# Performance work log

Measured on AMD Instinct MI355X. Metric: run time of the kernel, lower is better.

Reference implementation:

```python
import jax, jax.numpy as jnp
import numpy as np

FEAT = 512
HEADS = 8
HEAD_DIM = FEAT // HEADS
HIDDEN = 2048
EPS = 1e-5


def _linear(x, W, b):
    # torch Linear: y = x @ W.T + b, W: (out, in)
    return jnp.einsum('bnd,od->bno', x, W) + b


def _layernorm(x, g, b):
    mu = jnp.mean(x, axis=-1, keepdims=True)
    var = jnp.var(x, axis=-1, keepdims=True)
    return (x - mu) * jax.lax.rsqrt(var + EPS) * g + b


def setup_inputs() -> dict:
    key = jax.random.key(0)
    ks = jax.random.split(key, 16)
    bsz, N = 16, 512
    gain = 2 ** (-0.5)
    lim = gain * np.sqrt(6.0 / (FEAT + FEAT))
    inp = {
        'nfeat': jax.random.normal(ks[0], (bsz, N, FEAT), jnp.float32),
        'attn_bias': jax.random.normal(ks[1], (bsz, N, N, HEADS), jnp.float32),
        'attn_mask': jax.random.randint(ks[2], (bsz, N, N), 0, 2, jnp.int32),
        'Wq': jax.random.uniform(ks[3], (FEAT, FEAT), jnp.float32, -lim, lim),
        'bq': jnp.zeros((FEAT,), jnp.float32),
        'Wk': jax.random.uniform(ks[4], (FEAT, FEAT), jnp.float32, -lim, lim),
        'bk': jnp.zeros((FEAT,), jnp.float32),
        'Wv': jax.random.uniform(ks[5], (FEAT, FEAT), jnp.float32, -lim, lim),
        'bv': jnp.zeros((FEAT,), jnp.float32),
        'Wo': jax.random.uniform(ks[6], (FEAT, FEAT), jnp.float32, -np.sqrt(6.0/(2*FEAT)), np.sqrt(6.0/(2*FEAT))),
        'bo': jnp.zeros((FEAT,), jnp.float32),
        'W1': jax.random.normal(ks[7], (HIDDEN, FEAT), jnp.float32) * 0.02,
        'b1': jnp.zeros((HIDDEN,), jnp.float32),
        'W2': jax.random.normal(ks[8], (FEAT, HIDDEN), jnp.float32) * 0.02,
        'b2': jnp.zeros((FEAT,), jnp.float32),
        'ln1_g': jnp.ones((FEAT,), jnp.float32),
        'ln1_b': jnp.zeros((FEAT,), jnp.float32),
        'ln2_g': jnp.ones((FEAT,), jnp.float32),
        'ln2_b': jnp.zeros((FEAT,), jnp.float32),
    }
    return inp


def reference(nfeat, attn_bias, attn_mask, Wq, bq, Wk, bk, Wv, bv, Wo, bo,
              W1, b1, W2, b2, ln1_g, ln1_b, ln2_g, ln2_b):
    bsz, N, _ = nfeat.shape
    residual = nfeat
    # --- biased multi-head attention (norm_first=False => no pre-norm) ---
    q = _linear(nfeat, Wq, bq).reshape(bsz, N, HEADS, HEAD_DIM)
    k = _linear(nfeat, Wk, bk).reshape(bsz, N, HEADS, HEAD_DIM)
    v = _linear(nfeat, Wv, bv).reshape(bsz, N, HEADS, HEAD_DIM)
    # NOTE: original code does q / scaling with scaling = head_dim**-0.5,
    # i.e. scores are MULTIPLIED by sqrt(head_dim) (faithful to source).
    scale = jnp.float32(HEAD_DIM ** 0.5)
    scores = jnp.einsum('bqhd,bkhd->bhqk', q, k) * scale  # (b,h,N,N)
    scores = scores + jnp.transpose(attn_bias, (0, 3, 1, 2))  # additive bias
    mask = (attn_mask != 0)[:, None, :, :]
    scores = jnp.where(mask, -jnp.inf, scores)
    attn = jax.nn.softmax(scores, axis=-1)
    ctx = jnp.einsum('bhqk,bkhd->bqhd', attn, v).reshape(bsz, N, FEAT)
    out = _linear(ctx, Wo, bo)
    x = residual + out
    x = _layernorm(x, ln1_g, ln1_b)
    # --- FFN ---
    residual = x
    h = jax.nn.relu(_linear(x, W1, b1))
    h = _linear(h, W2, b2)
    x = residual + h
    x = _layernorm(x, ln2_g, ln2_b)
    return x
```

## Files before the change

kernel.cpp:

```cpp
#include <hip/hip_runtime.h>
#include <hip/hip_bf16.h>
#include <stdint.h>

typedef unsigned short u16;
typedef __attribute__((ext_vector_type(8))) __bf16 bf16x8;
typedef __attribute__((ext_vector_type(4))) float f32x4;
typedef __attribute__((ext_vector_type(4))) unsigned short u16x4;

#define B_   16
#define N_   512
#define D_   512
#define H_   8
#define DH_  64
#define HID_ 2048
#define M_   8192
#define FRAG_BH 32768

__device__ __forceinline__ u16 f2bf(float f) {
    unsigned u = __float_as_uint(f);
    u += 0x7fffu + ((u >> 16) & 1u);
    return (u16)(u >> 16);
}
__device__ __forceinline__ float bf2f(u16 u) {
    return __uint_as_float(((unsigned)u) << 16);
}
__device__ __forceinline__ f32x4 mfma16(bf16x8 a, bf16x8 b, f32x4 c) {
    return __builtin_amdgcn_mfma_f32_16x16x32_bf16(a, b, c, 0, 0, 0);
}
__device__ __forceinline__ void gload_lds16(const u16* g, u16* l) {
    __builtin_amdgcn_global_load_lds(
        (const __attribute__((address_space(1))) void*)g,
        (__attribute__((address_space(3))) void*)l, 16, 0, 0);
}

__device__ __forceinline__ void cvt4(const float* s, u16* d) {
    f32x4 v = *(const f32x4*)s;
    u16x4 o;
    o[0] = f2bf(v[0]); o[1] = f2bf(v[1]); o[2] = f2bf(v[2]); o[3] = f2bf(v[3]);
    *(u16x4*)d = o;
}
__device__ __forceinline__ void cvt4s(const float* s, u16* dh, u16* dl) {
    f32x4 v = *(const f32x4*)s;
    u16x4 oh, ol;
#pragma unroll
    for (int j = 0; j < 4; j++) {
        oh[j] = f2bf(v[j]);
        float r = v[j] - bf2f(oh[j]);
        ol[j] = f2bf(r);
    }
    *(u16x4*)dh = oh;
    *(u16x4*)dl = ol;
}

__global__ __launch_bounds__(256) void convert_all(
    const float* __restrict__ nf, const float* __restrict__ Wq,
    const float* __restrict__ Wk, const float* __restrict__ Wv,
    const float* __restrict__ Wo, const float* __restrict__ W1,
    const float* __restrict__ W2, const float* __restrict__ bq,
    const float* __restrict__ bk, const float* __restrict__ bv,
    u16* __restrict__ xh, u16* __restrict__ xl,
    u16* __restrict__ wqh, u16* __restrict__ wql,
    u16* __restrict__ wob, u16* __restrict__ w1b, u16* __restrict__ w2b,
    float* __restrict__ bqkv)
{
    long i = ((long)blockIdx.x * 256 + threadIdx.x) * 4;
    if (i < 4194304) { cvt4s(nf + i, xh + i, xl + i); return; }
    i -= 4194304;
    if (i < 786432) {
        const float* s = (i < 262144) ? (Wq + i)
                       : (i < 524288) ? (Wk + i - 262144) : (Wv + i - 524288);
        cvt4s(s, wqh + i, wql + i); return;
    }
    i -= 786432;
    if (i < 262144) { cvt4(Wo + i, wob + i); return; }
    i -= 262144;
    if (i < 1048576) { cvt4(W1 + i, w1b + i); return; }
    i -= 1048576;
    if (i < 1048576) { cvt4(W2 + i, w2b + i); return; }
    i -= 1048576;
    if (i < 1536) {
        const float* s = (i < 512) ? (bq + i) : (i < 1024 ? bk + i - 512 : bv + i - 1024);
        *(f32x4*)(bqkv + i) = *(const f32x4*)s;
    }
}

#define BM 128
#define BN 128
#define BK 32

__global__ __launch_bounds__(256) void gemm_qkv(
    const u16* __restrict__ Ah, const u16* __restrict__ Al,
    const u16* __restrict__ Wh, const u16* __restrict__ Wl,
    const float* __restrict__ bias,
    u16* __restrict__ Qf, u16* __restrict__ Qlf,
    u16* __restrict__ Kf, u16* __restrict__ Klf, u16* __restrict__ Vf)
{
    __shared__ u16 sAh[BM * BK], sAl[BM * BK], sBh[BN * BK], sBl[BN * BK];
    const int Kdim = 512;
    const int tid = threadIdx.x;
    const int w = tid >> 6, lane = tid & 63;
    const int lr = lane & 15, lg = lane >> 4;
    const int nTn = 1536 / BN;
    const int tm = blockIdx.x / nTn, tn = blockIdx.x % nTn;
    const long m0 = (long)tm * BM, n0 = (long)tn * BN;
    const int which = (int)(n0 >> 9);
    const bool vpath = (which == 2);

    f32x4 acc[4][4];
#pragma unroll
    for (int i = 0; i < 4; i++)
#pragma unroll
        for (int j = 0; j < 4; j++) acc[i][j] = (f32x4){0.f, 0.f, 0.f, 0.f};

    const int e0 = w * 512 + lane * 8;
    const int r0 = e0 >> 5, c0 = e0 & 31;
    const int r1 = r0 + 64;
    const long gA0 = (long)r0 * Kdim + c0, gA1 = (long)r1 * Kdim + c0;
    const u16* pAh = Ah + m0 * Kdim;
    const u16* pAl = Al + m0 * Kdim;
    const u16* pBh = Wh + n0 * Kdim;
    const u16* pBl = Wl + n0 * Kdim;
    u16* dAh0 = sAh + w * 512; u16* dAh1 = sAh + w * 512 + 2048;
    u16* dAl0 = sAl + w * 512; u16* dAl1 = sAl + w * 512 + 2048;
    u16* dBh0 = sBh + w * 512; u16* dBh1 = sBh + w * 512 + 2048;
    u16* dBl0 = sBl + w * 512; u16* dBl1 = sBl + w * 512 + 2048;

    const int wr = (w >> 1) * 64, wc = (w & 1) * 64;

    for (int k0 = 0; k0 < Kdim; k0 += BK) {
        gload_lds16(pAh + gA0 + k0, dAh0);
        gload_lds16(pAh + gA1 + k0, dAh1);
        gload_lds16(pBh + gA0 + k0, dBh0);
        gload_lds16(pBh + gA1 + k0, dBh1);
        if (!vpath) {
            gload_lds16(pAl + gA0 + k0, dAl0);
            gload_lds16(pAl + gA1 + k0, dAl1);
            gload_lds16(pBl + gA0 + k0, dBl0);
            gload_lds16(pBl + gA1 + k0, dBl1);
        }
        __syncthreads();
        bf16x8 ah[4], bh[4];
#pragma unroll
        for (int i = 0; i < 4; i++) {
            int ra = (wr + i * 16 + lr) * BK + lg * 8;
            int rb = (wc + i * 16 + lr) * BK + lg * 8;
            ah[i] = *reinterpret_cast<const bf16x8*>(&sAh[ra]);
            bh[i] = *reinterpret_cast<const bf16x8*>(&sBh[rb]);
        }
        if (vpath) {
#pragma unroll
            for (int i = 0; i < 4; i++)
#pragma unroll
                for (int j = 0; j < 4; j++)
                    acc[i][j] = mfma16(ah[i], bh[j], acc[i][j]);
        } else {
            bf16x8 al[4], bl[4];
#pragma unroll
            for (int i = 0; i < 4; i++) {
                int ra = (wr + i * 16 + lr) * BK + lg * 8;
                int rb = (wc + i * 16 + lr) * BK + lg * 8;
                al[i] = *reinterpret_cast<const bf16x8*>(&sAl[ra]);
                bl[i] = *reinterpret_cast<const bf16x8*>(&sBl[rb]);
            }
#pragma unroll
            for (int i = 0; i < 4; i++)
#pragma unroll
                for (int j = 0; j < 4; j++) {
                    acc[i][j] = mfma16(ah[i], bh[j], acc[i][j]);
                    acc[i][j] = mfma16(ah[i], bl[j], acc[i][j]);
                    acc[i][j] = mfma16(al[i], bh[j], acc[i][j]);
                }
        }
        __syncthreads();
    }

#pragma unroll
    for (int i = 0; i < 4; i++) {
#pragma unroll
        for (int j = 0; j < 4; j++) {
#pragma unroll
            for (int r = 0; r < 4; r++) {
                long m = m0 + wr + i * 16 + lg * 4 + r;
                long n = n0 + wc + j * 16 + lr;
                float v = acc[i][j][r] + bias[n];
                int b = (int)(m >> 9), nn = (int)(m & 511);
                int h = ((int)n >> 6) & 7, dh = (int)n & 63;
                long bh_ = (long)b * 8 + h;
                if (which == 2) {
                    int df = dh >> 4, rho = dh & 15;
                    int gam = (nn >> 3) & 3, e = nn & 7, nb32 = nn >> 5;
                    Vf[bh_ * FRAG_BH + (((long)nb32 * 4 + df) * 64 + gam * 16 + rho) * 8 + e]
                        = f2bf(v);
                } else {
                    int nb = nn >> 4, rho = nn & 15;
                    int kk = dh >> 5, gam = (dh >> 3) & 3, e = dh & 7;
                    long idx = bh_ * FRAG_BH + (((long)nb * 2 + kk) * 64 + gam * 16 + rho) * 8 + e;
                    u16 hi = f2bf(v);
                    u16 lo = f2bf(v - bf2f(hi));
                    if (which == 0) { Qf[idx] = hi; Qlf[idx] = lo; }
                    else            { Kf[idx] = hi; Klf[idx] = lo; }
                }
            }
        }
    }
}

template<int EPI>
__global__ __launch_bounds__(256) void gemm_bt(
    const u16* __restrict__ A, const u16* __restrict__ W,
    const float* __restrict__ bias, const float* __restrict__ resid,
    float* __restrict__ outf, u16* __restrict__ outb,
    int Mdim, int Ndim, int Kdim)
{
    __shared__ u16 As[BM * BK];
    __shared__ u16 Bs[BN * BK];
    const int tid = threadIdx.x;
    const int w = tid >> 6, lane = tid & 63;
    const int lr = lane & 15, lg = lane >> 4;
    const int nTn = Ndim / BN;
    const int tm = blockIdx.x / nTn, tn = blockIdx.x % nTn;
    const long m0 = (long)tm * BM, n0 = (long)tn * BN;

    f32x4 acc[4][4];
#pragma unroll
    for (int i = 0; i < 4; i++)
#pragma unroll
        for (int j = 0; j < 4; j++) acc[i][j] = (f32x4){0.f, 0.f, 0.f, 0.f};

    const int e0 = w * 512 + lane * 8;
    const int r0 = e0 >> 5, c0 = e0 & 31;
    const int r1 = r0 + 64, c1 = c0;
    u16* As0 = As + w * 512;
    u16* As1 = As + w * 512 + 2048;
    u16* Bs0 = Bs + w * 512;
    u16* Bs1 = Bs + w * 512 + 2048;
    const u16* Ag = A + m0 * Kdim;
    const u16* Bg = W + n0 * Kdim;

    const int wr = (w >> 1) * 64, wc = (w & 1) * 64;

    for (int k0 = 0; k0 < Kdim; k0 += BK) {
        gload_lds16(Ag + (long)r0 * Kdim + k0 + c0, As0);
        gload_lds16(Ag + (long)r1 * Kdim + k0 + c1, As1);
        gload_lds16(Bg + (long)r0 * Kdim + k0 + c0, Bs0);
        gload_lds16(Bg + (long)r1 * Kdim + k0 + c1, Bs1);
        __syncthreads();
        bf16x8 af[4], bfr[4];
#pragma unroll
        for (int i = 0; i < 4; i++) {
            af[i]  = *reinterpret_cast<const bf16x8*>(&As[(wr + i * 16 + lr) * BK + lg * 8]);
            bfr[i] = *reinterpret_cast<const bf16x8*>(&Bs[(wc + i * 16 + lr) * BK + lg * 8]);
        }
#pragma unroll
        for (int i = 0; i < 4; i++)
#pragma unroll
            for (int j = 0; j < 4; j++)
                acc[i][j] = mfma16(af[i], bfr[j], acc[i][j]);
        __syncthreads();
    }

#pragma unroll
    for (int i = 0; i < 4; i++) {
#pragma unroll
        for (int j = 0; j < 4; j++) {
#pragma unroll
            for (int r = 0; r < 4; r++) {
                long m = m0 + wr + i * 16 + lg * 4 + r;
                long n = n0 + wc + j * 16 + lr;
                float v = acc[i][j][r];
                if (EPI == 1) {
                    long idx = m * Ndim + n;
                    outf[idx] = v + bias[n] + resid[idx];
                } else {
                    float t = v + bias[n];
                    t = t > 0.f ? t : 0.f;
                    outb[m * Ndim + n] = f2bf(t);
                }
            }
        }
    }
}

#define PLST 1060
#define PST  72

__global__ __launch_bounds__(512) void attn_kernel(
    const u16* __restrict__ Qf, const u16* __restrict__ Qlf,
    const u16* __restrict__ Kf, const u16* __restrict__ Klf,
    const u16* __restrict__ Vf,
    const float* __restrict__ bias, const int* __restrict__ mask,
    u16* __restrict__ ctx)
{
    __shared__ float Bs[8 * PLST];
    __shared__ u16 Ps[8 * 16 * PST];
    const int tid = threadIdx.x;
    const int w = tid >> 6, lane = tid & 63;
    const int lr = lane & 15, lg = lane >> 4;
    const int b = blockIdx.x >> 5, qt = blockIdx.x & 31;
    const int bq0 = qt * 16;
    const long bh = (long)b * 8 + w;
    const u16* Qfp  = Qf  + bh * FRAG_BH;
    const u16* Qlfp = Qlf + bh * FRAG_BH;
    const u16* Kfp  = Kf  + bh * FRAG_BH;
    const u16* Klfp = Klf + bh * FRAG_BH;
    const u16* Vfp  = Vf  + bh * FRAG_BH;

    const int sq = tid >> 5, st = tid & 31;
    const float* bias_row = bias + ((long)b * 512 + bq0 + sq) * 512 * 8;
    const int*   mask_row = mask + ((long)b * 512 + bq0 + sq) * 512;

    bf16x8 qhf[2], qlf[2];
#pragma unroll
    for (int kk = 0; kk < 2; kk++) {
        long off = (((long)qt * 2 + kk) * 64 + lane) * 8;
        qhf[kk] = *reinterpret_cast<const bf16x8*>(&Qfp[off]);
        qlf[kk] = *reinterpret_cast<const bf16x8*>(&Qlfp[off]);
    }

    f32x4 of[4];
    float m_run[4], l_run[4];
#pragma unroll
    for (int df = 0; df < 4; df++) of[df] = (f32x4){0.f, 0.f, 0.f, 0.f};
#pragma unroll
    for (int r = 0; r < 4; r++) { m_run[r] = -1e30f; l_run[r] = 0.f; }

    float* Bw = Bs + w * PLST;
    u16* Pw = Ps + w * 16 * PST;

    f32x4 bA[4], bB[4];
    int mA[4], mB[4];

    auto loadbias = [&](int kt, f32x4 (&bb)[4], int (&mm)[4]) {
#pragma unroll
        for (int j = 0; j < 4; j++) {
            int f = st + j * 32;
            bb[j] = *(const f32x4*)(bias_row + (long)kt * 512 + f * 4);
            mm[j] = mask_row[kt * 64 + (f >> 1)];
        }
    };

    auto body = [&](int kt, f32x4 (&bc)[4], int (&mc)[4],
                    f32x4 (&bn)[4], int (&mn)[4], bool pf) {
        f32x4 s[4];
#pragma unroll
        for (int kf = 0; kf < 4; kf++) s[kf] = (f32x4){0.f, 0.f, 0.f, 0.f};
#pragma unroll
        for (int kf = 0; kf < 4; kf++) {
            long kb = (((long)(kt * 4 + kf) * 2) * 64 + lane) * 8;
            bf16x8 kh0 = *reinterpret_cast<const bf16x8*>(&Kfp[kb]);
            bf16x8 kh1 = *reinterpret_cast<const bf16x8*>(&Kfp[kb + 512]);
            bf16x8 kl0 = *reinterpret_cast<const bf16x8*>(&Klfp[kb]);
            bf16x8 kl1 = *reinterpret_cast<const bf16x8*>(&Klfp[kb + 512]);
            __builtin_amdgcn_s_setprio(1);
            s[kf] = mfma16(qhf[0], kh0, s[kf]);
            s[kf] = mfma16(qhf[1], kh1, s[kf]);
            s[kf] = mfma16(qhf[0], kl0, s[kf]);
            s[kf] = mfma16(qhf[1], kl1, s[kf]);
            s[kf] = mfma16(qlf[0], kh0, s[kf]);
            s[kf] = mfma16(qlf[1], kh1, s[kf]);
            __builtin_amdgcn_s_setprio(0);
        }
        __syncthreads();
#pragma unroll
        for (int j = 0; j < 4; j++) {
            int f = st + j * 32;
            int k = f >> 1, h4 = (f & 1) * 4;
            bool msk = (mc[j] != 0);
#pragma unroll
            for (int c = 0; c < 4; c++)
                Bs[(h4 + c) * PLST + sq * 66 + k] = msk ? -3e38f : bc[j][c];
        }
        __syncthreads();
        if (pf) loadbias(kt + 1, bn, mn);
#pragma unroll
        for (int r = 0; r < 4; r++) {
            int qrow = lg * 4 + r;
#pragma unroll
            for (int kf = 0; kf < 4; kf++)
                s[kf][r] = s[kf][r] * 8.0f + Bw[qrow * 66 + kf * 16 + lr];
        }
#pragma unroll
        for (int r = 0; r < 4; r++) {
            float pm = fmaxf(fmaxf(s[0][r], s[1][r]), fmaxf(s[2][r], s[3][r]));
            pm = fmaxf(pm, __shfl_xor(pm, 1));
            pm = fmaxf(pm, __shfl_xor(pm, 2));
            pm = fmaxf(pm, __shfl_xor(pm, 4));
            pm = fmaxf(pm, __shfl_xor(pm, 8));
            float mn_ = fmaxf(m_run[r], pm);
            float fac = __expf(m_run[r] - mn_);
            m_run[r] = mn_;
            float rs = 0.f;
#pragma unroll
            for (int kf = 0; kf < 4; kf++) {
                float p = __expf(s[kf][r] - mn_);
                s[kf][r] = p;
                rs += p;
            }
            rs += __shfl_xor(rs, 1); rs += __shfl_xor(rs, 2);
            rs += __shfl_xor(rs, 4); rs += __shfl_xor(rs, 8);
            l_run[r] = l_run[r] * fac + rs;
#pragma unroll
            for (int df = 0; df < 4; df++) of[df][r] *= fac;
        }
#pragma unroll
        for (int kf = 0; kf < 4; kf++)
#pragma unroll
            for (int r = 0; r < 4; r++)
                Pw[(lg * 4 + r) * PST + kf * 16 + lr] = f2bf(s[kf][r]);
#pragma unroll
        for (int kk = 0; kk < 2; kk++) {
            bf16x8 pa = *reinterpret_cast<const bf16x8*>(
                &Pw[lr * PST + kk * 32 + lg * 8]);
#pragma unroll
            for (int df = 0; df < 4; df++) {
                bf16x8 vb = *reinterpret_cast<const bf16x8*>(
                    &Vfp[((((long)(kt * 2 + kk)) * 4 + df) * 64 + lane) * 8]);
                __builtin_amdgcn_s_setprio(1);
                of[df] = mfma16(pa, vb, of[df]);
                __builtin_amdgcn_s_setprio(0);
            }
        }
    };

    loadbias(0, bA, mA);
#pragma unroll
    for (int kt2 = 0; kt2 < 4; kt2++) {
        body(kt2 * 2,     bA, mA, bB, mB, true);
        body(kt2 * 2 + 1, bB, mB, bA, mA, kt2 < 3);
    }

#pragma unroll
    for (int r = 0; r < 4; r++) {
        int q = bq0 + lg * 4 + r;
        float inv = 1.0f / l_run[r];
        u16* crow = ctx + ((long)b * 512 + q) * 512 + w * 64;
#pragma unroll
        for (int df = 0; df < 4; df++)
            crow[df * 16 + lr] = f2bf(of[df][r] * inv);
    }
}

template<int WB>
__global__ __launch_bounds__(256) void ln_kernel(
    const float* __restrict__ xin, const float* __restrict__ g,
    const float* __restrict__ bta, float* __restrict__ fout, u16* __restrict__ bout)
{
    const int tid = threadIdx.x;
    const int w = tid >> 6, lane = tid & 63;
    const long row = (long)blockIdx.x * 4 + w;
    const float* xp = xin + row * 512 + lane * 8;
    f32x4 v0 = *(const f32x4*)(xp);
    f32x4 v1 = *(const f32x4*)(xp + 4);
    float sum = v0[0] + v0[1] + v0[2] + v0[3] + v1[0] + v1[1] + v1[2] + v1[3];
    float sq = v0[0]*v0[0] + v0[1]*v0[1] + v0[2]*v0[2] + v0[3]*v0[3]
             + v1[0]*v1[0] + v1[1]*v1[1] + v1[2]*v1[2] + v1[3]*v1[3];
#pragma unroll
    for (int m = 1; m <= 32; m <<= 1) {
        sum += __shfl_xor(sum, m);
        sq  += __shfl_xor(sq, m);
    }
    float mu = sum * (1.f / 512.f);
    float var = sq * (1.f / 512.f) - mu * mu;
    float rstd = rsqrtf(var + 1e-5f);
#pragma unroll
    for (int j = 0; j < 8; j++) {
        int c = lane * 8 + j;
        float x = (j < 4) ? v0[j] : v1[j - 4];
        float y = (x - mu) * rstd * g[c] + bta[c];
        fout[row * 512 + c] = y;
        if (WB) bout[row * 512 + c] = f2bf(y);
    }
}

extern "C" void kernel_launch(void* const* d_in, const int* in_sizes, int n_in,
                              void* d_out, int out_size, void* d_ws, size_t ws_size,
                              hipStream_t stream)
{
    const float* nfeat     = (const float*)d_in[0];
    const float* attn_bias = (const float*)d_in[1];
    const int*   attn_mask = (const int*)d_in[2];
    const float* Wq = (const float*)d_in[3];
    const float* bq = (const float*)d_in[4];
    const float* Wk = (const float*)d_in[5];
    const float* bk = (const float*)d_in[6];
    const float* Wv = (const float*)d_in[7];
    const float* bv = (const float*)d_in[8];
    const float* Wo = (const float*)d_in[9];
    const float* bo = (const float*)d_in[10];
    const float* W1 = (const float*)d_in[11];
    const float* b1 = (const float*)d_in[12];
    const float* W2 = (const float*)d_in[13];
    const float* b2 = (const float*)d_in[14];
    const float* ln1_g = (const float*)d_in[15];
    const float* ln1_b = (const float*)d_in[16];
    const float* ln2_g = (const float*)d_in[17];
    const float* ln2_b = (const float*)d_in[18];

    char* ws = (char*)d_ws;
    size_t off = 0;
    auto alloc = [&](size_t bytes) -> void* {
        void* p = ws + off;
        off += (bytes + 255) & ~(size_t)255;
        return p;
    };
    u16* xh    = (u16*)alloc((size_t)M_ * D_ * 2);
    u16* xl    = (u16*)alloc((size_t)M_ * D_ * 2);
    u16* wqh   = (u16*)alloc((size_t)1536 * 512 * 2);
    u16* wql   = (u16*)alloc((size_t)1536 * 512 * 2);
    u16* wob   = (u16*)alloc((size_t)512 * 512 * 2);
    u16* w1b   = (u16*)alloc((size_t)2048 * 512 * 2);
    u16* w2b   = (u16*)alloc((size_t)512 * 2048 * 2);
    float* bqkv = (float*)alloc(1536 * 4);
    u16* Qf    = (u16*)alloc((size_t)128 * FRAG_BH * 2);
    u16* Qlf   = (u16*)alloc((size_t)128 * FRAG_BH * 2);
    u16* Kf    = (u16*)alloc((size_t)128 * FRAG_BH * 2);
    u16* Klf   = (u16*)alloc((size_t)128 * FRAG_BH * 2);
    u16* Vf    = (u16*)alloc((size_t)128 * FRAG_BH * 2);
    u16* ctx   = (u16*)alloc((size_t)M_ * D_ * 2);
    float* xres = (float*)alloc((size_t)M_ * D_ * 4);
    float* x1f  = (float*)alloc((size_t)M_ * D_ * 4);
    u16* x1b   = (u16*)alloc((size_t)M_ * D_ * 2);
    u16* hb    = (u16*)alloc((size_t)M_ * HID_ * 2);

    convert_all<<<7170, 256, 0, stream>>>(nfeat, Wq, Wk, Wv, Wo, W1, W2, bq, bk, bv,
                                          xh, xl, wqh, wql, wob, w1b, w2b, bqkv);
    gemm_qkv<<<(M_/BM) * (1536/BN), 256, 0, stream>>>(
        xh, xl, wqh, wql, bqkv, Qf, Qlf, Kf, Klf, Vf);
    attn_kernel<<<B_ * 32, 512, 0, stream>>>(
        Qf, Qlf, Kf, Klf, Vf, attn_bias, attn_mask, ctx);
    gemm_bt<1><<<(M_/BM) * (512/BN), 256, 0, stream>>>(
        ctx, wob, bo, nfeat, xres, nullptr, M_, 512, 512);
    ln_kernel<1><<<M_ / 4, 256, 0, stream>>>(xres, ln1_g, ln1_b, x1f, x1b);
    gemm_bt<2><<<(M_/BM) * (HID_/BN), 256, 0, stream>>>(
        x1b, w1b, b1, nullptr, nullptr, hb, M_, HID_, 512);
    gemm_bt<1><<<(M_/BM) * (512/BN), 256, 0, stream>>>(
        hb, w2b, b2, x1f, xres, nullptr, M_, 512, 2048);
    ln_kernel<0><<<M_ / 4, 256, 0, stream>>>(xres, ln2_g, ln2_b, (float*)d_out, nullptr);
}
```

Measured before the change: 504.2 us.

## Pre-transform attention bias and mask into bf16 MFMA fragment layout in a separate kernel

A new bias_prep kernel reads the fp32 attn_bias and int mask once, folds the mask in, converts to bf16 and writes the result in the per-head MFMA accumulator layout. The attention kernel then loads these fragments directly, dropping its LDS transpose buffer, two block-wide barriers per tile and the double-buffered bias prefetch. V fragments are also loaded up front each iteration. The cost is an extra kernel launch plus a write and re-read of a bf16 bias buffer, and rounding the bias to bf16 may affect accuracy, since scores are scaled by 8 and the bias is added afterwards.

```diff
diff --git a/kernel.cpp b/kernel.cpp
--- a/kernel.cpp
+++ b/kernel.cpp
@@ -6,6 +6,7 @@
 typedef __attribute__((ext_vector_type(8))) __bf16 bf16x8;
 typedef __attribute__((ext_vector_type(4))) float f32x4;
 typedef __attribute__((ext_vector_type(4))) unsigned short u16x4;
+typedef __attribute__((ext_vector_type(4))) int i32x4;
 
 #define B_   16
 #define N_   512
@@ -81,6 +82,45 @@
     if (i < 1536) {
         const float* s = (i < 512) ? (bq + i) : (i < 1024 ? bk + i - 512 : bv + i - 1024);
         *(f32x4*)(bqkv + i) = *(const f32x4*)s;
+    }
+}
+
+__global__ __launch_bounds__(512) void bias_prep(
+    const float* __restrict__ bias, const int* __restrict__ mask,
+    u16* __restrict__ biasF)
+{
+    __shared__ float Ls[8192];
+    __shared__ int Ms[1024];
+    const int tid = threadIdx.x;
+    const int bid = blockIdx.x;
+    const int kt = bid & 7, qt = (bid >> 3) & 31, b = bid >> 8;
+    const float* src = bias + (((long)b * 512 + qt * 16) * 512 + kt * 64) * 8;
+#pragma unroll
+    for (int i = 0; i < 4; i++) {
+        int lin = i * 2048 + tid * 4;
+        int q = lin >> 9, rem = lin & 511;
+        *(f32x4*)&Ls[lin] = *(const f32x4*)(src + (long)q * 4096 + rem);
+    }
+    if (tid < 256) {
+        int q = tid >> 4, k4 = (tid & 15) * 4;
+        const int* ms = mask + ((long)b * 512 + qt * 16 + q) * 512 + kt * 64 + k4;
+        *(i32x4*)&Ms[q * 64 + k4] = *(const i32x4*)ms;
+    }
+    __syncthreads();
+    const int w = tid >> 6, lane = tid & 63;
+    const int lr = lane & 15, lg = lane >> 4;
+    const long bh = (long)b * 8 + w;
+    u16* dst = biasF + (((bh * 32 + qt) * 8 + kt) * 4) * 256 + lane * 4;
+#pragma unroll
+    for (int kf = 0; kf < 4; kf++) {
+        u16x4 o;
+#pragma unroll
+        for (int r = 0; r < 4; r++) {
+            int q = lg * 4 + r, k = kf * 16 + lr;
+            float f = Ls[q * 512 + k * 8 + w];
+            o[r] = Ms[q * 64 + k] ? f2bf(-3e38f) : f2bf(f);
+        }
+        *(u16x4*)(dst + kf * 256) = o;
     }
 }
 
@@ -281,17 +321,14 @@
     }
 }
 
-#define PLST 1060
 #define PST  72
 
 __global__ __launch_bounds__(512) void attn_kernel(
     const u16* __restrict__ Qf, const u16* __restrict__ Qlf,
     const u16* __restrict__ Kf, const u16* __restrict__ Klf,
-    const u16* __restrict__ Vf,
-    const float* __restrict__ bias, const int* __restrict__ mask,
+    const u16* __restrict__ Vf, const u16* __restrict__ biasF,
     u16* __restrict__ ctx)
 {
-    __shared__ float Bs[8 * PLST];
     __shared__ u16 Ps[8 * 16 * PST];
     const int tid = threadIdx.x;
     const int w = tid >> 6, lane = tid & 63;
@@ -304,10 +341,7 @@
     const u16* Kfp  = Kf  + bh * FRAG_BH;
     const u16* Klfp = Klf + bh * FRAG_BH;
     const u16* Vfp  = Vf  + bh * FRAG_BH;
-
-    const int sq = tid >> 5, st = tid & 31;
-    const float* bias_row = bias + ((long)b * 512 + bq0 + sq) * 512 * 8;
-    const int*   mask_row = mask + ((long)b * 512 + bq0 + sq) * 512;
+    const u16* bFp  = biasF + ((bh * 32 + qt) * 8) * 1024 + lane * 4;
 
     bf16x8 qhf[2], qlf[2];
 #pragma unroll
@@ -324,23 +358,21 @@
 #pragma unroll
     for (int r = 0; r < 4; r++) { m_run[r] = -1e30f; l_run[r] = 0.f; }
 
-    float* Bw = Bs + w * PLST;
     u16* Pw = Ps + w * 16 * PST;
 
-    f32x4 bA[4], bB[4];
-    int mA[4], mB[4];
-
-    auto loadbias = [&](int kt, f32x4 (&bb)[4], int (&mm)[4]) {
-#pragma unroll
-        for (int j = 0; j < 4; j++) {
-            int f = st + j * 32;
-            bb[j] = *(const f32x4*)(bias_row + (long)kt * 512 + f * 4);
-            mm[j] = mask_row[kt * 64 + (f >> 1)];
-        }
-    };
-
-    auto body = [&](int kt, f32x4 (&bc)[4], int (&mc)[4],
-                    f32x4 (&bn)[4], int (&mn)[4], bool pf) {
+#pragma unroll
+    for (int kt = 0; kt < 8; kt++) {
+        u16x4 br[4];
+#pragma unroll
+        for (int kf = 0; kf < 4; kf++)
+            br[kf] = *(const u16x4*)(bFp + kt * 1024 + kf * 256);
+        bf16x8 vr[2][4];
+#pragma unroll
+        for (int kk = 0; kk < 2; kk++)
+#pragma unroll
+            for (int df = 0; df < 4; df++)
+                vr[kk][df] = *reinterpret_cast<const bf16x8*>(
+                    &Vfp[(((long)(kt * 2 + kk) * 4 + df) * 64 + lane) * 8]);
         f32x4 s[4];
 #pragma unroll
         for (int kf = 0; kf < 4; kf++) s[kf] = (f32x4){0.f, 0.f, 0.f, 0.f};
@@ -360,25 +392,11 @@
             s[kf] = mfma16(qlf[1], kh1, s[kf]);
             __builtin_amdgcn_s_setprio(0);
         }
-        __syncthreads();
-#pragma unroll
-        for (int j = 0; j < 4; j++) {
-            int f = st + j * 32;
-            int k = f >> 1, h4 = (f & 1) * 4;
-            bool msk = (mc[j] != 0);
-#pragma unroll
-            for (int c = 0; c < 4; c++)
-                Bs[(h4 + c) * PLST + sq * 66 + k] = msk ? -3e38f : bc[j][c];
-        }
-        __syncthreads();
-        if (pf) loadbias(kt + 1, bn, mn);
-#pragma unroll
-        for (int r = 0; r < 4; r++) {
-            int qrow = lg * 4 + r;
-#pragma unroll
-            for (int kf = 0; kf < 4; kf++)
-                s[kf][r] = s[kf][r] * 8.0f + Bw[qrow * 66 + kf * 16 + lr];
-        }
+#pragma unroll
+        for (int kf = 0; kf < 4; kf++)
+#pragma unroll
+            for (int r = 0; r < 4; r++)
+                s[kf][r] = s[kf][r] * 8.0f + bf2f(br[kf][r]);
 #pragma unroll
         for (int r = 0; r < 4; r++) {
             float pm = fmaxf(fmaxf(s[0][r], s[1][r]), fmaxf(s[2][r], s[3][r]));
@@ -411,22 +429,12 @@
         for (int kk = 0; kk < 2; kk++) {
             bf16x8 pa = *reinterpret_cast<const bf16x8*>(
                 &Pw[lr * PST + kk * 32 + lg * 8]);
-#pragma unroll
-            for (int df = 0; df < 4; df++) {
-                bf16x8 vb = *reinterpret_cast<const bf16x8*>(
-                    &Vfp[((((long)(kt * 2 + kk)) * 4 + df) * 64 + lane) * 8]);
-                __builtin_amdgcn_s_setprio(1);
-                of[df] = mfma16(pa, vb, of[df]);
-                __builtin_amdgcn_s_setprio(0);
-            }
-        }
-    };
-
-    loadbias(0, bA, mA);
-#pragma unroll
-    for (int kt2 = 0; kt2 < 4; kt2++) {
-        body(kt2 * 2,     bA, mA, bB, mB, true);
-        body(kt2 * 2 + 1, bB, mB, bA, mA, kt2 < 3);
+            __builtin_amdgcn_s_setprio(1);
+#pragma unroll
+            for (int df = 0; df < 4; df++)
+                of[df] = mfma16(pa, vr[kk][df], of[df]);
+            __builtin_amdgcn_s_setprio(0);
+        }
     }
 
 #pragma unroll
@@ -516,6 +524,7 @@
     u16* Kf    = (u16*)alloc((size_t)128 * FRAG_BH * 2);
     u16* Klf   = (u16*)alloc((size_t)128 * FRAG_BH * 2);
     u16* Vf    = (u16*)alloc((size_t)128 * FRAG_BH * 2);
+    u16* biasF = (u16*)alloc((size_t)128 * 32 * 8 * 4 * 64 * 4 * 2);
     u16* ctx   = (u16*)alloc((size_t)M_ * D_ * 2);
     float* xres = (float*)alloc((size_t)M_ * D_ * 4);
     float* x1f  = (float*)alloc((size_t)M_ * D_ * 4);
@@ -524,10 +533,11 @@
 
     convert_all<<<7170, 256, 0, stream>>>(nfeat, Wq, Wk, Wv, Wo, W1, W2, bq, bk, bv,
                                           xh, xl, wqh, wql, wob, w1b, w2b, bqkv);
+    bias_prep<<<16 * 32 * 8, 512, 0, stream>>>(attn_bias, attn_mask, biasF);
     gemm_qkv<<<(M_/BM) * (1536/BN), 256, 0, stream>>>(
         xh, xl, wqh, wql, bqkv, Qf, Qlf, Kf, Klf, Vf);
     attn_kernel<<<B_ * 32, 512, 0, stream>>>(
-        Qf, Qlf, Kf, Klf, Vf, attn_bias, attn_mask, ctx);
+        Qf, Qlf, Kf, Klf, Vf, biasF, ctx);
     gemm_bt<1><<<(M_/BM) * (512/BN), 256, 0, stream>>>(
         ctx, wob, bo, nfeat, xres, nullptr, M_, 512, 512);
     ln_kernel<1><<<M_ / 4, 256, 0, stream>>>(xres, ln1_g, ln1_b, x1f, x1b);
```

After: 523.0 us. 3.7% more time.
